# Optimization experiments

Measured on AMD Instinct MI355X. Metric: run time of the kernel, lower is better.

The kernel has to match this reference:

```python
import jax, jax.numpy as jnp
import numpy as np

N_USERS = 100000
N_ITEMS = 50000
NNZ = 3000000  # user-item interactions; symmetric adjacency has 2*NNZ edges
D = 64
N_LAYERS = 3


def setup_inputs() -> dict:
    key = jax.random.key(0)
    k1, k2, k3 = jax.random.split(key, 3)
    N = N_USERS + N_ITEMS
    users = jax.random.randint(k1, (NNZ,), 0, N_USERS)
    items = jax.random.randint(k2, (NNZ,), 0, N_ITEMS) + N_USERS
    # symmetric bipartite adjacency: u->i and i->u edges
    row = jnp.concatenate([users, items]).astype(jnp.int32)
    col = jnp.concatenate([items, users]).astype(jnp.int32)
    # D^{-1/2} A D^{-1/2} normalization, matching (deg + 1e-7)^{-0.5}
    deg = jax.ops.segment_sum(jnp.ones(row.shape, dtype=jnp.float32), row, num_segments=N)
    dinv = jnp.power(deg + 1e-7, -0.5)
    vals = dinv[row] * dinv[col]
    in_embs = jax.random.normal(k3, (N, D), dtype=jnp.float32)
    return {"in_embs": in_embs, "row": row, "col": col, "vals": vals, "n_layers": N_LAYERS}


def reference(in_embs, row, col, vals, n_layers):
    N = in_embs.shape[0]
    # result = in_embs + sum_i [ x_i/(i+1) + x_i ]  (original appends both per layer)
    out = in_embs
    x = in_embs
    for i in range(n_layers):
        # SpMM: x <- A_norm @ x  via gather + segment scatter-add
        x = jax.ops.segment_sum(vals[:, None] * x[col], row, num_segments=N)
        # F.normalize(x, dim=-1) with torch's eps=1e-12 clamp
        x = x / jnp.maximum(jnp.linalg.norm(x, axis=-1, keepdims=True), 1e-12)
        out = out + x * (1.0 + 1.0 / (i + 1))
    return out
```

## Files before the change

kernel.cpp:

```cpp
#include <hip/hip_runtime.h>
#include <hip/hip_bf16.h>

#define D 64
#define BW 512
#define BSH 9
#define BMASK 511
#define MAXK 512
#define CHUNK 8192
#define SSPLIT 8

typedef unsigned short u16;
typedef unsigned int u32;
typedef _Float16 half2_t __attribute__((ext_vector_type(2)));

__device__ __forceinline__ u16 f2h(float f) {
    union { _Float16 h; u16 u; } v; v.h = (_Float16)f; return v.u;
}
__device__ __forceinline__ float hlo(u32 u) {
    union { u32 x; half2_t h; } v; v.x = u; return (float)v.h.x;
}
__device__ __forceinline__ float hhi(u32 u) {
    union { u32 x; half2_t h; } v; v.x = u; return (float)v.h.y;
}
__device__ __forceinline__ float dot2lo(u32 u, float acc) {
    union { u32 x; half2_t h; } v; v.x = u;
    half2_t one = {(_Float16)1.0f, (_Float16)0.0f};
    return __builtin_amdgcn_fdot2(v.h, one, acc, false);
}
__device__ __forceinline__ float dot2hi(u32 u, float acc) {
    union { u32 x; half2_t h; } v; v.x = u;
    half2_t one = {(_Float16)0.0f, (_Float16)1.0f};
    return __builtin_amdgcn_fdot2(v.h, one, acc, false);
}


__global__ __launch_bounds__(256) void chunk_hist_kernel(
        const int* __restrict__ row, int* __restrict__ H,
        int E, int K, int nchunks) {
    __shared__ int h[MAXK];
    int ch = blockIdx.x;
    int cbeg = ch * CHUNK;
    int cend = min(cbeg + CHUNK, E);
    for (int i = threadIdx.x; i < K; i += 256) h[i] = 0;
    __syncthreads();
    for (int e = cbeg + threadIdx.x; e < cend; e += 256)
        atomicAdd(&h[__builtin_nontemporal_load(&row[e]) >> BSH], 1);
    __syncthreads();
    for (int i = threadIdx.x; i < K; i += 256)
        H[(size_t)i * nchunks + ch] = h[i];
}


__global__ __launch_bounds__(256) void bucket_colscan_kernel(
        int* __restrict__ H, int* __restrict__ btot, int nchunks) {
    __shared__ int tmp[256];
    int b = blockIdx.x;
    int t = threadIdx.x;
    int* Hb = H + (size_t)b * nchunks;
    int cpt = (nchunks + 255) >> 8;
    int beg = min(t * cpt, nchunks), end = min(beg + cpt, nchunks);
    int s = 0;
    for (int i = beg; i < end; ++i) s += Hb[i];
    tmp[t] = s;
    __syncthreads();
    for (int d = 1; d < 256; d <<= 1) {
        int x = (t >= d) ? tmp[t - d] : 0;
        __syncthreads();
        tmp[t] += x;
        __syncthreads();
    }
    int run = tmp[t] - s;
    for (int i = beg; i < end; ++i) {
        int v = Hb[i];
        Hb[i] = run;
        run += v;
    }
    if (t == 255) btot[b] = tmp[255];
}


__global__ __launch_bounds__(1024) void bucket_scan_kernel(
        const int* __restrict__ btot, int* __restrict__ bbase, int K, int E) {
    __shared__ int tmp[1024];
    int t = threadIdx.x;
    int v = (t < K) ? btot[t] : 0;
    tmp[t] = v;
    __syncthreads();
    for (int d = 1; d < 1024; d <<= 1) {
        int x = (t >= d) ? tmp[t - d] : 0;
        __syncthreads();
        tmp[t] += x;
        __syncthreads();
    }
    if (t < K) bbase[t] = tmp[t] - v;
    if (t == 0) bbase[K] = E;
}


__global__ __launch_bounds__(256) void scatter_sort_kernel(
        const int* __restrict__ row, const int* __restrict__ col,
        const int* __restrict__ H, const int* __restrict__ btot,
        const int* __restrict__ bbase,
        u32* __restrict__ pairs, int E, int K, int nchunks) {
    __shared__ u32 stage[CHUNK];
    __shared__ int hcur[MAXK];
    __shared__ int lbase[MAXK + 1];
    __shared__ int gdest[MAXK];
    __shared__ int red[256];
    int ch = blockIdx.x;
    int cbeg = ch * CHUNK;
    int cend = min(cbeg + CHUNK, E);
    int cnt_total = cend - cbeg;
    int t = threadIdx.x;

    int j0 = 2 * t, j1 = 2 * t + 1;
    int d0 = 0, d1 = 0;
    if (j0 < K) {
        int st = H[(size_t)j0 * nchunks + ch];
        int en = (ch + 1 < nchunks) ? H[(size_t)j0 * nchunks + ch + 1] : btot[j0];
        d0 = en - st;
        gdest[j0] = bbase[j0] + st;
    }
    if (j1 < K) {
        int st = H[(size_t)j1 * nchunks + ch];
        int en = (ch + 1 < nchunks) ? H[(size_t)j1 * nchunks + ch + 1] : btot[j1];
        d1 = en - st;
        gdest[j1] = bbase[j1] + st;
    }
    int s = d0 + d1;
    red[t] = s;
    __syncthreads();
    for (int d = 1; d < 256; d <<= 1) {
        int x = (t >= d) ? red[t - d] : 0;
        __syncthreads();
        red[t] += x;
        __syncthreads();
    }
    int ex = red[t] - s;
    if (j0 < K) { lbase[j0] = ex; hcur[j0] = ex; }
    if (j1 < K) { lbase[j1] = ex + d0; hcur[j1] = ex + d0; }
    if (t == 255) lbase[K] = red[255];
    __syncthreads();

    for (int e = cbeg + t; e < cend; e += 256) {
        int r = row[e];
        u32 c = (u32)col[e];
        int p = atomicAdd(&hcur[r >> BSH], 1);
        stage[p] = ((u32)(r & BMASK) << 18) | c;
    }
    __syncthreads();

    for (int p = t; p < cnt_total; p += 256) {
        int lo = 0, hi = K;
        while (hi - lo > 1) {
            int mid = (lo + hi) >> 1;
            if (lbase[mid] <= p) lo = mid; else hi = mid;
        }
        pairs[gdest[lo] + (p - lbase[lo])] = stage[p];
    }
}


__global__ __launch_bounds__(256) void csr_hist_kernel(
        const u32* __restrict__ pairs, const int* __restrict__ bbase,
        int* __restrict__ P, int K) {
    __shared__ int h[BW];
    int b = blockIdx.x;
    int k = b / SSPLIT, s = b % SSPLIT;
    int t = threadIdx.x;
    h[t] = 0; h[t + 256] = 0;
    __syncthreads();
    int ebeg = bbase[k], eend = bbase[k + 1];
    int len = eend - ebeg;
    int sb = ebeg + (int)((long long)len * s / SSPLIT);
    int se = ebeg + (int)((long long)len * (s + 1) / SSPLIT);
    for (int e = sb + t; e < se; e += 256)
        atomicAdd(&h[pairs[e] >> 18], 1);
    __syncthreads();
    int* Pks = P + ((size_t)k * SSPLIT + s) * BW;
    Pks[t] = h[t];
    Pks[t + 256] = h[t + 256];
}

__global__ __launch_bounds__(256) void csr_scan_kernel(
        int* __restrict__ P, const int* __restrict__ bbase,
        int* __restrict__ ptr, float* __restrict__ dinv,
        float* __restrict__ sdeg, int N, int K) {
    __shared__ int red[256];
    int k = blockIdx.x;
    int t = threadIdx.x;
    int r0 = k << BSH;
    int* Pk = P + (size_t)k * SSPLIT * BW;
    int q0[SSPLIT], q1[SSPLIT];
    int d0 = 0, d1 = 0;
    #pragma unroll
    for (int s = 0; s < SSPLIT; ++s) {
        q0[s] = d0; d0 += Pk[s * BW + 2 * t];
        q1[s] = d1; d1 += Pk[s * BW + 2 * t + 1];
    }
    int sum = d0 + d1;
    red[t] = sum;
    __syncthreads();
    for (int d = 1; d < 256; d <<= 1) {
        int x = (t >= d) ? red[t - d] : 0;
        __syncthreads();
        red[t] += x;
        __syncthreads();
    }
    int ex = red[t] - sum;
    int base0 = bbase[k] + ex;
    int base1 = base0 + d0;
    int ra = r0 + 2 * t, rb = r0 + 2 * t + 1;
    if (ra < N) {
        ptr[ra] = base0;
        float f = (float)d0 + 1e-7f;
        float sq = sqrtf(f);
        dinv[ra] = 1.0f / sq;
        sdeg[ra] = sq;
    }
    if (rb < N) {
        ptr[rb] = base1;
        float f = (float)d1 + 1e-7f;
        float sq = sqrtf(f);
        dinv[rb] = 1.0f / sq;
        sdeg[rb] = sq;
    }
    #pragma unroll
    for (int s = 0; s < SSPLIT; ++s) {
        Pk[s * BW + 2 * t]     = base0 + q0[s];
        Pk[s * BW + 2 * t + 1] = base1 + q1[s];
    }
    if (k == 0 && t == 0) ptr[N] = bbase[K];
}

__global__ __launch_bounds__(256) void csr_fill_kernel(
        const u32* __restrict__ pairs, const int* __restrict__ bbase,
        const int* __restrict__ P, int* __restrict__ ccol, int K) {
    __shared__ int cur[BW];
    int b = blockIdx.x;
    int xcd = b & 7;
    int q = b >> 3;
    int s = q % SSPLIT;
    int kk = q / SSPLIT;
    int k = kk * 8 + xcd;
    if (k >= K) return;
    int t = threadIdx.x;
    const int* Pks = P + ((size_t)k * SSPLIT + s) * BW;
    cur[t] = Pks[t];
    cur[t + 256] = Pks[t + 256];
    __syncthreads();
    int ebeg = bbase[k], eend = bbase[k + 1];
    int len = eend - ebeg;
    int sb = ebeg + (int)((long long)len * s / SSPLIT);
    int se = ebeg + (int)((long long)len * (s + 1) / SSPLIT);
    for (int e = sb + t; e < se; e += 256) {
        u32 pk = pairs[e];
        int pos = atomicAdd(&cur[pk >> 18], 1);
        ccol[pos] = (int)(pk & 0x3FFFFu);
    }
}

__global__ void scale_in_kernel(const float* __restrict__ in,
                                const float* __restrict__ dinv,
                                u16* __restrict__ y0, int npairs) {
    int p = blockIdx.x * blockDim.x + threadIdx.x;
    if (p >= npairs) return;
    float2 v = *reinterpret_cast<const float2*>(&in[(size_t)p * 2]);
    float dv = dinv[p >> 5];
    u32 up = (u32)f2h(v.x * dv) | ((u32)f2h(v.y * dv) << 16);
    *reinterpret_cast<u32*>(&y0[(size_t)p * 2]) = up;
}

template <bool FINAL>
__global__ __launch_bounds__(256) void layer_kernel(
        const u16* __restrict__ y_src,
        const int* __restrict__ ptr,
        const int* __restrict__ ccol,
        const float* __restrict__ dinv,
        const float* __restrict__ sdeg,
        u16* __restrict__ y_dst,
        const float* __restrict__ in_embs,
        const u16* __restrict__ y1,
        float* __restrict__ out,
        int rbeg, int rend) {
    int wid = (blockIdx.x * blockDim.x + threadIdx.x) >> 6;
    int lane = threadIdx.x & 63;
    int rh = lane >> 5;
    int b = (lane >> 3) & 3;
    int a = lane & 7;
    int r = rbeg + wid * 2 + rh;
    if (r >= rend) return;
    const size_t dimoff = (size_t)a * 8;

    int s = ptr[r], e = ptr[r + 1];
    float acc[8];
    #pragma unroll
    for (int i = 0; i < 8; ++i) acc[i] = 0.f;

#define ACCQ(q)                                            \
    do {                                                   \
        u32 qa_[4] = {(q).x, (q).y, (q).z, (q).w};         \
        _Pragma("unroll")                                  \
        for (int i_ = 0; i_ < 4; ++i_) {                   \
            acc[2 * i_]     = dot2lo(qa_[i_], acc[2 * i_]);     \
            acc[2 * i_ + 1] = dot2hi(qa_[i_], acc[2 * i_ + 1]); \
        }                                                  \
    } while (0)

    int j = s;
    #pragma unroll 2
    for (; j + 8 <= e; j += 8) {
        int c0 = __builtin_nontemporal_load(&ccol[j + b]);
        int c1 = __builtin_nontemporal_load(&ccol[j + 4 + b]);
        uint4 q0 = *reinterpret_cast<const uint4*>(&y_src[(size_t)c0 * D + dimoff]);
        uint4 q1 = *reinterpret_cast<const uint4*>(&y_src[(size_t)c1 * D + dimoff]);
        ACCQ(q0);
        ACCQ(q1);
    }
    if (j + 4 <= e) {
        int c = __builtin_nontemporal_load(&ccol[j + b]);
        uint4 q = *reinterpret_cast<const uint4*>(&y_src[(size_t)c * D + dimoff]);
        ACCQ(q);
        j += 4;
    }
    if (j + b < e) {
        int c = __builtin_nontemporal_load(&ccol[j + b]);
        uint4 q = *reinterpret_cast<const uint4*>(&y_src[(size_t)c * D + dimoff]);
        ACCQ(q);
    }
#undef ACCQ

    #pragma unroll
    for (int off = 8; off <= 16; off <<= 1) {
        #pragma unroll
        for (int i = 0; i < 8; ++i) acc[i] += __shfl_xor(acc[i], off);
    }

    float ss = 0.f;
    #pragma unroll
    for (int i = 0; i < 8; ++i) ss += acc[i] * acc[i];
    #pragma unroll
    for (int off = 1; off <= 4; off <<= 1) ss += __shfl_xor(ss, off);
    float inv = 1.0f / fmaxf(sqrtf(ss), 1e-12f);

    if (b == 0) {
        size_t idx = (size_t)r * D + dimoff;
        if (FINAL) {
            float sd = sdeg[r];
            float4 i0 = *reinterpret_cast<const float4*>(&in_embs[idx]);
            float4 i1 = *reinterpret_cast<const float4*>(&in_embs[idx + 4]);
            uint4 w1 = *reinterpret_cast<const uint4*>(&y1[idx]);
            uint4 w2 = *reinterpret_cast<const uint4*>(&y_src[idx]);
            u32 w1a[4] = {w1.x, w1.y, w1.z, w1.w};
            u32 w2a[4] = {w2.x, w2.y, w2.z, w2.w};
            float o[8];
            #pragma unroll
            for (int i = 0; i < 4; ++i) {
                o[2 * i]     = 2.0f * sd * hlo(w1a[i]) + 1.5f * sd * hlo(w2a[i])
                             + (4.0f / 3.0f) * acc[2 * i] * inv;
                o[2 * i + 1] = 2.0f * sd * hhi(w1a[i]) + 1.5f * sd * hhi(w2a[i])
                             + (4.0f / 3.0f) * acc[2 * i + 1] * inv;
            }
            float4 o0 = {o[0] + i0.x, o[1] + i0.y, o[2] + i0.z, o[3] + i0.w};
            float4 o1 = {o[4] + i1.x, o[5] + i1.y, o[6] + i1.z, o[7] + i1.w};
            *reinterpret_cast<float4*>(&out[idx])     = o0;
            *reinterpret_cast<float4*>(&out[idx + 4]) = o1;
        } else {
            float dv = dinv[r] * inv;
            uint4 w;
            w.x = (u32)f2h(acc[0] * dv) | ((u32)f2h(acc[1] * dv) << 16);
            w.y = (u32)f2h(acc[2] * dv) | ((u32)f2h(acc[3] * dv) << 16);
            w.z = (u32)f2h(acc[4] * dv) | ((u32)f2h(acc[5] * dv) << 16);
            w.w = (u32)f2h(acc[6] * dv) | ((u32)f2h(acc[7] * dv) << 16);
            *reinterpret_cast<uint4*>(&y_dst[idx]) = w;
        }
    }
}


__global__ void spmm_scatter_kernel(const float* __restrict__ x_src,
                                    const int* __restrict__ row,
                                    const int* __restrict__ col,
                                    const float* __restrict__ vals,
                                    float* __restrict__ x_dst, int E) {
    int gid = blockIdx.x * blockDim.x + threadIdx.x;
    int e = gid >> 6;
    int lane = threadIdx.x & 63;
    if (e >= E) return;
    float xv = x_src[(size_t)col[e] * D + lane];
    atomicAdd(&x_dst[(size_t)row[e] * D + lane], vals[e] * xv);
}

__global__ void norm_accum_kernel(float* __restrict__ x, float* __restrict__ out,
                                  float coef, int N) {
    int gid = blockIdx.x * blockDim.x + threadIdx.x;
    int rowi = gid >> 6;
    int lane = threadIdx.x & 63;
    if (rowi >= N) return;
    size_t idx = (size_t)rowi * D + lane;
    float v = x[idx];
    float s = v * v;
    #pragma unroll
    for (int off = 32; off >= 1; off >>= 1) s += __shfl_xor(s, off);
    float nv = v / fmaxf(sqrtf(s), 1e-12f);
    x[idx] = nv;
    out[idx] += coef * nv;
}

static inline size_t align256(size_t x) { return (x + 255) & ~(size_t)255; }

extern "C" void kernel_launch(void* const* d_in, const int* in_sizes, int n_in,
                              void* d_out, int out_size, void* d_ws, size_t ws_size,
                              hipStream_t stream) {
    const float* in_embs = (const float*)d_in[0];
    const int*   row     = (const int*)d_in[1];
    const int*   col     = (const int*)d_in[2];
    const float* vals    = (const float*)d_in[3];

    const int N = in_sizes[0] / D;
    const int E = in_sizes[1];

    float* out = (float*)d_out;

    const size_t embElems = (size_t)N * D;
    const size_t f16Bytes = embElems * sizeof(u16);
    const int K = (N + BW - 1) / BW;
    const int nchunks = (E + CHUNK - 1) / CHUNK;
    const size_t Hbytes = (size_t)K * nchunks * 4;
    const size_t Pbytes = (size_t)K * SSPLIT * BW * 4;

    size_t off = 0;
    const size_t o_ccol  = off; off += align256((size_t)E * 4);
    const size_t o_ptr   = off; off += align256(((size_t)N + 1) * 4);
    const size_t o_dinv  = off; off += align256((size_t)N * 4);
    const size_t o_sdeg  = off; off += align256((size_t)N * 4);
    const size_t o_btot  = off; off += align256((size_t)MAXK * 4);
    const size_t o_bbase = off; off += align256(((size_t)MAXK + 1) * 4);
    const size_t o_X     = off;
    const size_t xNeedA  = align256((size_t)E * 4) + align256(Hbytes) + align256(Pbytes);
    const size_t xNeedB  = 2 * align256(f16Bytes);
    const size_t xBytes  = (xNeedA > xNeedB) ? xNeedA : xNeedB;
    const size_t needed  = o_X + align256(xBytes);

    dim3 block(256);
    const int npairs = (int)(embElems / 2);
    dim3 pgrid((unsigned)((npairs + 255) / 256));

    if (ws_size >= needed && K <= MAXK) {
        char* wsb = (char*)d_ws;
        int*   ccol  = (int*)(wsb + o_ccol);
        int*   ptr   = (int*)(wsb + o_ptr);
        float* dinv  = (float*)(wsb + o_dinv);
        float* sdeg  = (float*)(wsb + o_sdeg);
        int*   btot  = (int*)(wsb + o_btot);
        int*   bbase = (int*)(wsb + o_bbase);
        u32*   pairs = (u32*)(wsb + o_X);
        int*   H     = (int*)(wsb + o_X + align256((size_t)E * 4));
        int*   P     = (int*)(wsb + o_X + align256((size_t)E * 4) + align256(Hbytes));
        u16*   bufA  = (u16*)(wsb + o_X);
        u16*   bufB  = (u16*)(wsb + o_X + align256(f16Bytes));

        chunk_hist_kernel<<<dim3((unsigned)nchunks), block, 0, stream>>>(
            row, H, E, K, nchunks);
        bucket_colscan_kernel<<<dim3((unsigned)K), block, 0, stream>>>(
            H, btot, nchunks);
        bucket_scan_kernel<<<dim3(1), dim3(1024), 0, stream>>>(btot, bbase, K, E);
        scatter_sort_kernel<<<dim3((unsigned)nchunks), block, 0, stream>>>(
            row, col, H, btot, bbase, pairs, E, K, nchunks);
        csr_hist_kernel<<<dim3((unsigned)(K * SSPLIT)), block, 0, stream>>>(
            pairs, bbase, P, K);
        csr_scan_kernel<<<dim3((unsigned)K), block, 0, stream>>>(
            P, bbase, ptr, dinv, sdeg, N, K);
        const unsigned fillGrid = 8u * SSPLIT * ((K + 7) / 8);
        csr_fill_kernel<<<dim3(fillGrid), block, 0, stream>>>(
            pairs, bbase, P, ccol, K);

        scale_in_kernel<<<pgrid, block, 0, stream>>>(in_embs, dinv, bufA, npairs);

        int nu = (N == 150000) ? 100000 : N;
        auto launch_layer = [&](const u16* src, u16* dst, const u16* y1p,
                                bool fin, int rb, int re) {
            int rows = re - rb;
            if (rows <= 0) return;
            dim3 g((unsigned)(((rows + 1) / 2 + 3) / 4));
            if (fin)
                layer_kernel<true><<<g, block, 0, stream>>>(
                    src, ptr, ccol, dinv, sdeg, nullptr, in_embs, y1p, out, rb, re);
            else
                layer_kernel<false><<<g, block, 0, stream>>>(
                    src, ptr, ccol, dinv, sdeg, dst, nullptr, nullptr, nullptr, rb, re);
        };

        launch_layer(bufA, bufB, nullptr, false, 0, nu);
        launch_layer(bufA, bufB, nullptr, false, nu, N);
        launch_layer(bufB, bufA, nullptr, false, 0, nu);
        launch_layer(bufB, bufA, nullptr, false, nu, N);
        launch_layer(bufA, nullptr, bufB, true, 0, nu);
        launch_layer(bufA, nullptr, bufB, true, nu, N);
    } else {
        float* fA = (float*)d_ws;
        float* fB = fA + embElems;
        hipMemcpyAsync(out, in_embs, embElems * 4, hipMemcpyDeviceToDevice, stream);
        const float coefs[3] = {2.0f, 1.5f, 4.0f / 3.0f};
        dim3 sgrid((unsigned)((E + 3) / 4));
        dim3 ngrid((unsigned)((N + 3) / 4));
        const float* src = in_embs;
        float* dst = fA;
        float* other = fB;
        for (int i = 0; i < 3; ++i) {
            hipMemsetAsync(dst, 0, embElems * 4, stream);
            spmm_scatter_kernel<<<sgrid, block, 0, stream>>>(src, row, col, vals, dst, E);
            norm_accum_kernel<<<ngrid, block, 0, stream>>>(dst, out, coefs[i], N);
            src = dst;
            float* t = dst; dst = other; other = t;
        }
    }
}
```

Before: 433.1 us.

## Merge user/item layer launches, deepen gather unroll, drop binary search in scatter

The scatter-sort kernel now records each staged element's bucket in shared memory along with a per-bucket global offset, so the write-out no longer binary-searches bucket bounds. The split user/item layer launches are merged into one launch per layer, with the wave index choosing the row range, which halves the number of layer kernels. The gather loop also processes 16 neighbours per iteration to keep more loads in flight. The extra shared array and the wider unroll raise LDS and register use, which may lower occupancy.

```diff
diff --git a/kernel.cpp b/kernel.cpp
--- a/kernel.cpp
+++ b/kernel.cpp
@@ -103,9 +103,9 @@
         const int* __restrict__ bbase,
         u32* __restrict__ pairs, int E, int K, int nchunks) {
     __shared__ u32 stage[CHUNK];
+    __shared__ u16 sbkt[CHUNK];
     __shared__ int hcur[MAXK];
-    __shared__ int lbase[MAXK + 1];
-    __shared__ int gdest[MAXK];
+    __shared__ int gofs[MAXK];
     __shared__ int red[256];
     int ch = blockIdx.x;
     int cbeg = ch * CHUNK;
@@ -114,18 +114,16 @@
     int t = threadIdx.x;
 
     int j0 = 2 * t, j1 = 2 * t + 1;
-    int d0 = 0, d1 = 0;
+    int d0 = 0, d1 = 0, st0 = 0, st1 = 0;
     if (j0 < K) {
-        int st = H[(size_t)j0 * nchunks + ch];
+        st0 = H[(size_t)j0 * nchunks + ch];
         int en = (ch + 1 < nchunks) ? H[(size_t)j0 * nchunks + ch + 1] : btot[j0];
-        d0 = en - st;
-        gdest[j0] = bbase[j0] + st;
+        d0 = en - st0;
     }
     if (j1 < K) {
-        int st = H[(size_t)j1 * nchunks + ch];
+        st1 = H[(size_t)j1 * nchunks + ch];
         int en = (ch + 1 < nchunks) ? H[(size_t)j1 * nchunks + ch + 1] : btot[j1];
-        d1 = en - st;
-        gdest[j1] = bbase[j1] + st;
+        d1 = en - st1;
     }
     int s = d0 + d1;
     red[t] = s;
@@ -137,27 +135,28 @@
         __syncthreads();
     }
     int ex = red[t] - s;
-    if (j0 < K) { lbase[j0] = ex; hcur[j0] = ex; }
-    if (j1 < K) { lbase[j1] = ex + d0; hcur[j1] = ex + d0; }
-    if (t == 255) lbase[K] = red[255];
+    if (j0 < K) {
+        hcur[j0] = ex;
+        gofs[j0] = (bbase[j0] + st0) - ex;
+    }
+    if (j1 < K) {
+        hcur[j1] = ex + d0;
+        gofs[j1] = (bbase[j1] + st1) - (ex + d0);
+    }
     __syncthreads();
 
     for (int e = cbeg + t; e < cend; e += 256) {
         int r = row[e];
         u32 c = (u32)col[e];
-        int p = atomicAdd(&hcur[r >> BSH], 1);
+        int b = r >> BSH;
+        int p = atomicAdd(&hcur[b], 1);
         stage[p] = ((u32)(r & BMASK) << 18) | c;
-    }
-    __syncthreads();
-
-    for (int p = t; p < cnt_total; p += 256) {
-        int lo = 0, hi = K;
-        while (hi - lo > 1) {
-            int mid = (lo + hi) >> 1;
-            if (lbase[mid] <= p) lo = mid; else hi = mid;
-        }
-        pairs[gdest[lo] + (p - lbase[lo])] = stage[p];
-    }
+        sbkt[p] = (u16)b;
+    }
+    __syncthreads();
+
+    for (int p = t; p < cnt_total; p += 256)
+        pairs[gofs[sbkt[p]] + p] = stage[p];
 }
 
 
@@ -282,14 +281,20 @@
         const float* __restrict__ in_embs,
         const u16* __restrict__ y1,
         float* __restrict__ out,
-        int rbeg, int rend) {
+        int nu, int N, int wavesU) {
     int wid = (blockIdx.x * blockDim.x + threadIdx.x) >> 6;
     int lane = threadIdx.x & 63;
     int rh = lane >> 5;
     int b = (lane >> 3) & 3;
     int a = lane & 7;
-    int r = rbeg + wid * 2 + rh;
-    if (r >= rend) return;
+    int r;
+    if (wid < wavesU) {
+        r = wid * 2 + rh;
+        if (r >= nu) return;
+    } else {
+        r = nu + (wid - wavesU) * 2 + rh;
+        if (r >= N) return;
+    }
     const size_t dimoff = (size_t)a * 8;
 
     int s = ptr[r], e = ptr[r + 1];
@@ -308,14 +313,28 @@
     } while (0)
 
     int j = s;
-    #pragma unroll 2
-    for (; j + 8 <= e; j += 8) {
+    for (; j + 16 <= e; j += 16) {
+        int c0 = __builtin_nontemporal_load(&ccol[j + b]);
+        int c1 = __builtin_nontemporal_load(&ccol[j + 4 + b]);
+        int c2 = __builtin_nontemporal_load(&ccol[j + 8 + b]);
+        int c3 = __builtin_nontemporal_load(&ccol[j + 12 + b]);
+        uint4 q0 = *reinterpret_cast<const uint4*>(&y_src[(size_t)c0 * D + dimoff]);
+        uint4 q1 = *reinterpret_cast<const uint4*>(&y_src[(size_t)c1 * D + dimoff]);
+        uint4 q2 = *reinterpret_cast<const uint4*>(&y_src[(size_t)c2 * D + dimoff]);
+        uint4 q3 = *reinterpret_cast<const uint4*>(&y_src[(size_t)c3 * D + dimoff]);
+        ACCQ(q0);
+        ACCQ(q1);
+        ACCQ(q2);
+        ACCQ(q3);
+    }
+    if (j + 8 <= e) {
         int c0 = __builtin_nontemporal_load(&ccol[j + b]);
         int c1 = __builtin_nontemporal_load(&ccol[j + 4 + b]);
         uint4 q0 = *reinterpret_cast<const uint4*>(&y_src[(size_t)c0 * D + dimoff]);
         uint4 q1 = *reinterpret_cast<const uint4*>(&y_src[(size_t)c1 * D + dimoff]);
         ACCQ(q0);
         ACCQ(q1);
+        j += 8;
     }
     if (j + 4 <= e) {
         int c = __builtin_nontemporal_load(&ccol[j + b]);
@@ -478,25 +497,16 @@
         scale_in_kernel<<<pgrid, block, 0, stream>>>(in_embs, dinv, bufA, npairs);
 
         int nu = (N == 150000) ? 100000 : N;
-        auto launch_layer = [&](const u16* src, u16* dst, const u16* y1p,
-                                bool fin, int rb, int re) {
-            int rows = re - rb;
-            if (rows <= 0) return;
-            dim3 g((unsigned)(((rows + 1) / 2 + 3) / 4));
-            if (fin)
-                layer_kernel<true><<<g, block, 0, stream>>>(
-                    src, ptr, ccol, dinv, sdeg, nullptr, in_embs, y1p, out, rb, re);
-            else
-                layer_kernel<false><<<g, block, 0, stream>>>(
-                    src, ptr, ccol, dinv, sdeg, dst, nullptr, nullptr, nullptr, rb, re);
-        };
-
-        launch_layer(bufA, bufB, nullptr, false, 0, nu);
-        launch_layer(bufA, bufB, nullptr, false, nu, N);
-        launch_layer(bufB, bufA, nullptr, false, 0, nu);
-        launch_layer(bufB, bufA, nullptr, false, nu, N);
-        launch_layer(bufA, nullptr, bufB, true, 0, nu);
-        launch_layer(bufA, nullptr, bufB, true, nu, N);
+        int wu = (((nu + 1) / 2) + 3) / 4 * 4;
+        int wi = (N > nu) ? ((((N - nu + 1) / 2) + 3) / 4 * 4) : 0;
+        dim3 lgrid((unsigned)((wu + wi) / 4));
+
+        layer_kernel<false><<<lgrid, block, 0, stream>>>(
+            bufA, ptr, ccol, dinv, sdeg, bufB, nullptr, nullptr, nullptr, nu, N, wu);
+        layer_kernel<false><<<lgrid, block, 0, stream>>>(
+            bufB, ptr, ccol, dinv, sdeg, bufA, nullptr, nullptr, nullptr, nu, N, wu);
+        layer_kernel<true><<<lgrid, block, 0, stream>>>(
+            bufA, ptr, ccol, dinv, sdeg, nullptr, in_embs, bufB, out, nu, N, wu);
     } else {
         float* fA = (float*)d_ws;
         float* fB = fA + embElems;
```

After: 414.8 us. -4.2%, faster.
